# Kernel optimization log

Measured on AMD Instinct MI355X. Metric: run time of the kernel, lower is better.

## Reference

```python
import jax, jax.numpy as jnp
import numpy as np

B, IN, H = 8192, 1024, 1024

def setup_inputs() -> dict:
    key = jax.random.key(0)
    ks = jax.random.split(key, 12)
    s_i = 1.0 / np.sqrt(IN)   # lecun-normal-ish scale for input kernels
    s_h = 1.0 / np.sqrt(H)
    d = {
        'inputs': jax.random.normal(ks[0], (B, IN), jnp.float32),
        'c': jax.random.normal(ks[1], (B, H), jnp.float32),
        'h': jax.random.normal(ks[2], (B, H), jnp.float32),
    }
    for n, k in zip(['Wii', 'Wif', 'Wig', 'Wio'], ks[3:7]):
        d[n] = jax.random.normal(k, (IN, H), jnp.float32) * s_i
    for n, k in zip(['Whi', 'Whf', 'Whg', 'Who'], ks[7:11]):
        d[n] = jax.random.normal(k, (H, H), jnp.float32) * s_h
    for n in ['bi', 'bf', 'bg', 'bo']:
        d[n] = jnp.zeros((H,), jnp.float32)
    return d

def reference(inputs, c, h, Wii, Wif, Wig, Wio, Whi, Whf, Whg, Who, bi, bf, bg, bo):
    # i = sigmoid(x Wii + h Whi + bi); f, o likewise; g = tanh(x Wig + h Whg + bg)
    i = jax.nn.sigmoid(inputs @ Wii + h @ Whi + bi)
    f = jax.nn.sigmoid(inputs @ Wif + h @ Whf + bf)
    g = jnp.tanh(inputs @ Wig + h @ Whg + bg)
    o = jax.nn.sigmoid(inputs @ Wio + h @ Who + bo)
    new_c = f * c + i * g
    new_h = o * jnp.tanh(new_c)
    return (new_c, new_h)
```

## Files before the change

### kernel.cpp

```cpp
#include <hip/hip_runtime.h>
#include <hip/hip_bf16.h>
#include <cstdint>


#define B_DIM 8192
#define H_DIM 1024
#define K2    2048
#define N4    4096

typedef __bf16 bf16x8 __attribute__((ext_vector_type(8)));
typedef __bf16 bf16x4 __attribute__((ext_vector_type(4)));
typedef float  f32x4  __attribute__((ext_vector_type(4)));

__device__ __forceinline__ void async_load16(const __bf16* g, __bf16* l) {
  __builtin_amdgcn_global_load_lds(
      (__attribute__((address_space(1))) void*)(g),
      (__attribute__((address_space(3))) void*)(l),
      16, 0, 0);
}

__device__ __forceinline__ float sigm(float x) {
  return 1.0f / (1.0f + __expf(-x));
}
__device__ __forceinline__ float tanh_fast(float x) {
  return 2.0f / (1.0f + __expf(-2.0f * x)) - 1.0f;
}

__global__ void cast_a(const float* __restrict__ x, const float* __restrict__ h,
                       __bf16* __restrict__ A) {
  int tid = blockIdx.x * blockDim.x + threadIdx.x;
  int row = tid >> 9;
  int k   = (tid & 511) << 2;
  const float* src = (k < H_DIM) ? (x + (size_t)row * H_DIM + k)
                                 : (h + (size_t)row * H_DIM + (k - H_DIM));
  float4 v = *(const float4*)src;
  bf16x4 o;
  o.x = (__bf16)v.x; o.y = (__bf16)v.y; o.z = (__bf16)v.z; o.w = (__bf16)v.w;
  *(bf16x4*)&A[(size_t)row * K2 + k] = o;
}

__global__ void cast_w(const float* __restrict__ Wii, const float* __restrict__ Wif,
                       const float* __restrict__ Wig, const float* __restrict__ Wio,
                       const float* __restrict__ Whi, const float* __restrict__ Whf,
                       const float* __restrict__ Whg, const float* __restrict__ Who,
                       __bf16* __restrict__ Bt) {
  __shared__ float tile[32][33];
  int k0 = blockIdx.x * 32;
  int j0 = blockIdx.y * 32;
  int gate = blockIdx.z;
  const float* Wi[4] = {Wii, Wif, Wig, Wio};
  const float* Wh[4] = {Whi, Whf, Whg, Who};
  const float* W = (k0 < H_DIM) ? Wi[gate] : Wh[gate];
  int kb = (k0 < H_DIM) ? k0 : (k0 - H_DIM);

  int tx = threadIdx.x & 31;
  int ty = threadIdx.x >> 5;
  for (int kk = ty; kk < 32; kk += 8)
    tile[kk][tx] = W[(size_t)(kb + kk) * H_DIM + j0 + tx];
  __syncthreads();
  for (int jj = ty; jj < 32; jj += 8) {
    int j = j0 + jj;
    int p = ((j >> 4) << 6) + (gate << 4) + (j & 15);
    Bt[(size_t)p * K2 + k0 + tx] = (__bf16)tile[tx][jj];
  }
}

__global__ __launch_bounds__(256) void lstm_gemm(
    const __bf16* __restrict__ A,
    const __bf16* __restrict__ Bt,
    const float* __restrict__ c,
    const float* __restrict__ bi, const float* __restrict__ bf_,
    const float* __restrict__ bg, const float* __restrict__ bo,
    float* __restrict__ out_c, float* __restrict__ out_h) {
  __shared__ __align__(16) __bf16 As[128 * 32];
  __shared__ __align__(16) __bf16 Bs[128 * 32];

  const int tid  = threadIdx.x;
  const int wave = tid >> 6;
  const int lane = tid & 63;
  const int wm   = wave >> 1;
  const int wn   = wave & 1;
  const int m0   = blockIdx.x * 128;
  const int n0   = blockIdx.y * 128;

  f32x4 acc[4][4] = {};

  const int l15  = lane & 15;
  const int quad = lane >> 4;
  const int kseg = quad * 8;

  const int srow0 = wave * 32 + (lane >> 2);
  const int srow1 = srow0 + 16;
  const int sseg  = (lane & 3) * 8;
  const __bf16* gA0 = A  + (size_t)(m0 + srow0) * K2 + sseg;
  const __bf16* gA1 = A  + (size_t)(m0 + srow1) * K2 + sseg;
  const __bf16* gB0 = Bt + (size_t)(n0 + srow0) * K2 + sseg;
  const __bf16* gB1 = Bt + (size_t)(n0 + srow1) * K2 + sseg;
  __bf16* lA0 = &As[(wave * 2 + 0) * 512];
  __bf16* lA1 = &As[(wave * 2 + 1) * 512];
  __bf16* lB0 = &Bs[(wave * 2 + 0) * 512];
  __bf16* lB1 = &Bs[(wave * 2 + 1) * 512];

  for (int k0 = 0; k0 < K2; k0 += 32) {
    __syncthreads();
    async_load16(gA0 + k0, lA0);
    async_load16(gA1 + k0, lA1);
    async_load16(gB0 + k0, lB0);
    async_load16(gB1 + k0, lB1);
    __syncthreads();

    bf16x8 af[4], bf8[4];
#pragma unroll
    for (int t = 0; t < 4; ++t)
      af[t] = *(const bf16x8*)&As[(wm * 64 + t * 16 + l15) * 32 + kseg];
#pragma unroll
    for (int t = 0; t < 4; ++t)
      bf8[t] = *(const bf16x8*)&Bs[(wn * 64 + t * 16 + l15) * 32 + kseg];

#pragma unroll
    for (int tm = 0; tm < 4; ++tm)
#pragma unroll
      for (int tn = 0; tn < 4; ++tn)
        acc[tm][tn] = __builtin_amdgcn_mfma_f32_16x16x32_bf16(
            af[tm], bf8[tn], acc[tm][tn], 0, 0, 0);
  }

  const int j = blockIdx.y * 32 + wn * 16 + l15;
  const float vbi = bi[j], vbf = bf_[j], vbg = bg[j], vbo = bo[j];

#pragma unroll
  for (int tm = 0; tm < 4; ++tm) {
#pragma unroll
    for (int r = 0; r < 4; ++r) {
      int row = m0 + wm * 64 + tm * 16 + quad * 4 + r;
      float gi = sigm(acc[tm][0][r] + vbi);
      float gf = sigm(acc[tm][1][r] + vbf);
      float gg = tanh_fast(acc[tm][2][r] + vbg);
      float go = sigm(acc[tm][3][r] + vbo);
      size_t idx = (size_t)row * H_DIM + j;
      float cv = c[idx];
      float nc = gf * cv + gi * gg;
      float nh = go * tanh_fast(nc);
      out_c[idx] = nc;
      out_h[idx] = nh;
    }
  }
}

extern "C" void kernel_launch(void* const* d_in, const int* in_sizes, int n_in,
                              void* d_out, int out_size, void* d_ws, size_t ws_size,
                              hipStream_t stream) {
  const float* x   = (const float*)d_in[0];
  const float* c   = (const float*)d_in[1];
  const float* h   = (const float*)d_in[2];
  const float* Wii = (const float*)d_in[3];
  const float* Wif = (const float*)d_in[4];
  const float* Wig = (const float*)d_in[5];
  const float* Wio = (const float*)d_in[6];
  const float* Whi = (const float*)d_in[7];
  const float* Whf = (const float*)d_in[8];
  const float* Whg = (const float*)d_in[9];
  const float* Who = (const float*)d_in[10];
  const float* bi  = (const float*)d_in[11];
  const float* bf_ = (const float*)d_in[12];
  const float* bg  = (const float*)d_in[13];
  const float* bo  = (const float*)d_in[14];

  __bf16* Abf = (__bf16*)d_ws;
  __bf16* Bt  = (__bf16*)((char*)d_ws + (size_t)B_DIM * K2 * 2);

  float* out_c = (float*)d_out;
  float* out_h = out_c + (size_t)B_DIM * H_DIM;

  cast_a<<<(B_DIM * K2 / 4) / 256, 256, 0, stream>>>(x, h, Abf);
  dim3 gw(K2 / 32, H_DIM / 32, 4);
  cast_w<<<gw, 256, 0, stream>>>(Wii, Wif, Wig, Wio, Whi, Whf, Whg, Who, Bt);
  dim3 gg(B_DIM / 128, N4 / 128);
  lstm_gemm<<<gg, 256, 0, stream>>>(Abf, Bt, c, bi, bf_, bg, bo, out_c, out_h);
}
```

Before: 396.3 us.

## Double GEMM K-tile to 64 with XOR-swizzled LDS and widen cast stores

```diff
diff --git a/kernel.cpp b/kernel.cpp
--- a/kernel.cpp
+++ b/kernel.cpp
@@ -7,6 +7,7 @@
 #define H_DIM 1024
 #define K2    2048
 #define N4    4096
+#define BK    64
 
 typedef __bf16 bf16x8 __attribute__((ext_vector_type(8)));
 typedef __bf16 bf16x4 __attribute__((ext_vector_type(4)));
@@ -28,15 +29,16 @@
 
 __global__ void cast_a(const float* __restrict__ x, const float* __restrict__ h,
                        __bf16* __restrict__ A) {
-  int tid = blockIdx.x * blockDim.x + threadIdx.x;
-  int row = tid >> 9;
-  int k   = (tid & 511) << 2;
+  int row = blockIdx.x;
+  int k = threadIdx.x << 3;
   const float* src = (k < H_DIM) ? (x + (size_t)row * H_DIM + k)
                                  : (h + (size_t)row * H_DIM + (k - H_DIM));
-  float4 v = *(const float4*)src;
-  bf16x4 o;
-  o.x = (__bf16)v.x; o.y = (__bf16)v.y; o.z = (__bf16)v.z; o.w = (__bf16)v.w;
-  *(bf16x4*)&A[(size_t)row * K2 + k] = o;
+  float4 v0 = *(const float4*)src;
+  float4 v1 = *(const float4*)(src + 4);
+  bf16x8 o;
+  o[0] = (__bf16)v0.x; o[1] = (__bf16)v0.y; o[2] = (__bf16)v0.z; o[3] = (__bf16)v0.w;
+  o[4] = (__bf16)v1.x; o[5] = (__bf16)v1.y; o[6] = (__bf16)v1.z; o[7] = (__bf16)v1.w;
+  *(bf16x8*)&A[(size_t)row * K2 + k] = o;
 }
 
 __global__ void cast_w(const float* __restrict__ Wii, const float* __restrict__ Wif,
@@ -58,11 +60,17 @@
   for (int kk = ty; kk < 32; kk += 8)
     tile[kk][tx] = W[(size_t)(kb + kk) * H_DIM + j0 + tx];
   __syncthreads();
-  for (int jj = ty; jj < 32; jj += 8) {
-    int j = j0 + jj;
-    int p = ((j >> 4) << 6) + (gate << 4) + (j & 15);
-    Bt[(size_t)p * K2 + k0 + tx] = (__bf16)tile[tx][jj];
-  }
+
+  int jj = threadIdx.x >> 3;
+  int kq = threadIdx.x & 7;
+  int j = j0 + jj;
+  int p = ((j >> 4) << 6) + (gate << 4) + (j & 15);
+  bf16x4 o;
+  o[0] = (__bf16)tile[kq * 4 + 0][jj];
+  o[1] = (__bf16)tile[kq * 4 + 1][jj];
+  o[2] = (__bf16)tile[kq * 4 + 2][jj];
+  o[3] = (__bf16)tile[kq * 4 + 3][jj];
+  *(bf16x4*)&Bt[(size_t)p * K2 + k0 + kq * 4] = o;
 }
 
 __global__ __launch_bounds__(256) void lstm_gemm(
@@ -72,8 +80,8 @@
     const float* __restrict__ bi, const float* __restrict__ bf_,
     const float* __restrict__ bg, const float* __restrict__ bo,
     float* __restrict__ out_c, float* __restrict__ out_h) {
-  __shared__ __align__(16) __bf16 As[128 * 32];
-  __shared__ __align__(16) __bf16 Bs[128 * 32];
+  __shared__ __align__(16) __bf16 As[128 * BK];
+  __shared__ __align__(16) __bf16 Bs[128 * BK];
 
   const int tid  = threadIdx.x;
   const int wave = tid >> 6;
@@ -87,42 +95,48 @@
 
   const int l15  = lane & 15;
   const int quad = lane >> 4;
-  const int kseg = quad * 8;
 
-  const int srow0 = wave * 32 + (lane >> 2);
-  const int srow1 = srow0 + 16;
-  const int sseg  = (lane & 3) * 8;
-  const __bf16* gA0 = A  + (size_t)(m0 + srow0) * K2 + sseg;
-  const __bf16* gA1 = A  + (size_t)(m0 + srow1) * K2 + sseg;
-  const __bf16* gB0 = Bt + (size_t)(n0 + srow0) * K2 + sseg;
-  const __bf16* gB1 = Bt + (size_t)(n0 + srow1) * K2 + sseg;
-  __bf16* lA0 = &As[(wave * 2 + 0) * 512];
-  __bf16* lA1 = &As[(wave * 2 + 1) * 512];
-  __bf16* lB0 = &Bs[(wave * 2 + 0) * 512];
-  __bf16* lB1 = &Bs[(wave * 2 + 1) * 512];
+  const int rin  = lane >> 3;
+  const int slot = lane & 7;
+  const int sg   = slot ^ rin;
+  const __bf16* gA[4]; const __bf16* gB[4];
+  __bf16* lA[4]; __bf16* lB[4];
+#pragma unroll
+  for (int c2 = 0; c2 < 4; ++c2) {
+    int r = wave * 32 + c2 * 8 + rin;
+    gA[c2] = A  + (size_t)(m0 + r) * K2 + sg * 8;
+    gB[c2] = Bt + (size_t)(n0 + r) * K2 + sg * 8;
+    lA[c2] = &As[(wave * 4 + c2) * 512];
+    lB[c2] = &Bs[(wave * 4 + c2) * 512];
+  }
 
-  for (int k0 = 0; k0 < K2; k0 += 32) {
+  for (int k0 = 0; k0 < K2; k0 += BK) {
     __syncthreads();
-    async_load16(gA0 + k0, lA0);
-    async_load16(gA1 + k0, lA1);
-    async_load16(gB0 + k0, lB0);
-    async_load16(gB1 + k0, lB1);
+#pragma unroll
+    for (int c2 = 0; c2 < 4; ++c2) async_load16(gA[c2] + k0, lA[c2]);
+#pragma unroll
+    for (int c2 = 0; c2 < 4; ++c2) async_load16(gB[c2] + k0, lB[c2]);
     __syncthreads();
 
-    bf16x8 af[4], bf8[4];
 #pragma unroll
-    for (int t = 0; t < 4; ++t)
-      af[t] = *(const bf16x8*)&As[(wm * 64 + t * 16 + l15) * 32 + kseg];
+    for (int kk = 0; kk < 2; ++kk) {
+      bf16x8 af[4], bfr[4];
+      const int want = kk * 4 + quad;
+      const int sw   = (want ^ (l15 & 7)) * 8;
 #pragma unroll
-    for (int t = 0; t < 4; ++t)
-      bf8[t] = *(const bf16x8*)&Bs[(wn * 64 + t * 16 + l15) * 32 + kseg];
+      for (int t = 0; t < 4; ++t)
+        af[t] = *(const bf16x8*)&As[(wm * 64 + t * 16 + l15) * BK + sw];
+#pragma unroll
+      for (int t = 0; t < 4; ++t)
+        bfr[t] = *(const bf16x8*)&Bs[(wn * 64 + t * 16 + l15) * BK + sw];
 
 #pragma unroll
-    for (int tm = 0; tm < 4; ++tm)
+      for (int tm = 0; tm < 4; ++tm)
 #pragma unroll
-      for (int tn = 0; tn < 4; ++tn)
-        acc[tm][tn] = __builtin_amdgcn_mfma_f32_16x16x32_bf16(
-            af[tm], bf8[tn], acc[tm][tn], 0, 0, 0);
+        for (int tn = 0; tn < 4; ++tn)
+          acc[tm][tn] = __builtin_amdgcn_mfma_f32_16x16x32_bf16(
+              af[tm], bfr[tn], acc[tm][tn], 0, 0, 0);
+    }
   }
 
   const int j = blockIdx.y * 32 + wn * 16 + l15;
@@ -172,7 +186,7 @@
   float* out_c = (float*)d_out;
   float* out_h = out_c + (size_t)B_DIM * H_DIM;
 
-  cast_a<<<(B_DIM * K2 / 4) / 256, 256, 0, stream>>>(x, h, Abf);
+  cast_a<<<B_DIM, 256, 0, stream>>>(x, h, Abf);
   dim3 gw(K2 / 32, H_DIM / 32, 4);
   cast_w<<<gw, 256, 0, stream>>>(Wii, Wif, Wig, Wio, Whi, Whf, Whg, Who, Bt);
   dim3 gg(B_DIM / 128, N4 / 128);
```

Measured after the change: 367.2 us. 7.3% less time.
